# Optimization experiments

Measured on AMD Instinct MI355X. Metric: run time of the kernel, lower is better.

The kernel has to match this reference:

```python
import jax, jax.numpy as jnp
import numpy as np
from jax import lax

Z_DIM = 64
ZS_SIZE = [[1, 1]] * 12 + [[2, 1]] + [[2, 2]] * 11 + [[4, 2]] + [[4, 4]] * 11  # 36 embeddings
FILTER = [[16, 16]] * 6 + [[16, 32]] + [[32, 32]] * 5 + [[32, 64]] + [[64, 64]] * 5  # 18 blocks
OFFS = np.cumsum([0] + [h * k for h, k in ZS_SIZE]).tolist()  # 242 z-vectors total


def _hyper(Z, hn_w2, hn_b2, hn_w1, hn_b1):
    # Batched HyperNetwork: Z [n, 64] -> kernels [n, 16, 16, 3, 3]
    n = Z.shape[0]
    h_in = (Z @ hn_w2 + hn_b2).reshape(n, 16, Z_DIM)            # [n, 16, 64]
    h_fin = jnp.einsum('nid,do->nio', h_in, hn_w1) + hn_b1       # [n, 16, 144]
    return h_fin.reshape(n, 16, 16, 3, 3)


def _make_w(z_all, idx, hn_w2, hn_b2, hn_w1, hn_b1):
    # Assemble conv weight [h*16, k*16, 3, 3] from h*k hypernet tiles (cat dim=1 over k, dim=0 over h)
    h, k = ZS_SIZE[idx]
    Z = z_all[OFFS[idx]:OFFS[idx] + h * k]
    K = _hyper(Z, hn_w2, hn_b2, hn_w1, hn_b1)                    # [h*k, 16, 16, 3, 3]
    K = K.reshape(h, k, 16, 16, 3, 3).transpose(0, 2, 1, 3, 4, 5)
    return K.reshape(h * 16, k * 16, 3, 3)


def _conv(x, w, stride, pad):
    return lax.conv_general_dilated(x, w, (stride, stride), [(pad, pad), (pad, pad)],
                                    dimension_numbers=('NCHW', 'OIHW', 'NCHW'))


def _bn(x, i, g, b, m, v):
    # eval-mode BatchNorm2d with running stats; params padded to 64 channels
    C = x.shape[1]
    gg = g[i, :C].reshape(1, C, 1, 1)
    bb = b[i, :C].reshape(1, C, 1, 1)
    mm = m[i, :C].reshape(1, C, 1, 1)
    vv = v[i, :C].reshape(1, C, 1, 1)
    return (x - mm) * (gg * lax.rsqrt(vv + 1e-5)) + bb


def setup_inputs() -> dict:
    key = jax.random.key(0)
    ks = jax.random.split(key, 16)
    B = 1024
    x = jax.random.normal(ks[0], (B, 3, 32, 32), jnp.float32)
    conv1_w = jax.random.normal(ks[1], (16, 3, 3, 3), jnp.float32) / np.float32(np.sqrt(27.0))
    conv1_b = jnp.zeros((16,), jnp.float32)
    n_bn = 37  # bn1 + 2 per block
    bn_gamma = jnp.ones((n_bn, 64), jnp.float32)
    bn_beta = jnp.zeros((n_bn, 64), jnp.float32)
    bn_mean = jnp.zeros((n_bn, 64), jnp.float32)
    bn_var = jnp.ones((n_bn, 64), jnp.float32)
    hn_w2 = jax.random.normal(ks[2], (Z_DIM, 16 * Z_DIM), jnp.float32) * 0.04
    hn_b2 = jax.random.normal(ks[3], (16 * Z_DIM,), jnp.float32) * 0.01
    hn_w1 = jax.random.normal(ks[4], (Z_DIM, 16 * 9), jnp.float32) * 0.04
    hn_b1 = jax.random.normal(ks[5], (16 * 9,), jnp.float32) * 0.01
    z_all = jax.random.normal(ks[6], (OFFS[-1], Z_DIM), jnp.float32)
    res_w6 = jax.random.normal(ks[7], (32, 16, 1, 1), jnp.float32) * 0.25
    res_b6 = jnp.zeros((32,), jnp.float32)
    res_w12 = jax.random.normal(ks[8], (64, 32, 1, 1), jnp.float32) * 0.18
    res_b12 = jnp.zeros((64,), jnp.float32)
    fin_w = jax.random.normal(ks[9], (10, 64), jnp.float32) * 0.1
    fin_b = jnp.zeros((10,), jnp.float32)
    return {"x": x, "conv1_w": conv1_w, "conv1_b": conv1_b,
            "bn_gamma": bn_gamma, "bn_beta": bn_beta, "bn_mean": bn_mean, "bn_var": bn_var,
            "hn_w2": hn_w2, "hn_b2": hn_b2, "hn_w1": hn_w1, "hn_b1": hn_b1,
            "z_all": z_all, "res_w6": res_w6, "res_b6": res_b6,
            "res_w12": res_w12, "res_b12": res_b12, "fin_w": fin_w, "fin_b": fin_b}


def reference(x, conv1_w, conv1_b, bn_gamma, bn_beta, bn_mean, bn_var,
              hn_w2, hn_b2, hn_w1, hn_b1, z_all,
              res_w6, res_b6, res_w12, res_b12, fin_w, fin_b):
    x = _conv(x, conv1_w, 1, 1) + conv1_b.reshape(1, -1, 1, 1)
    x = jax.nn.relu(_bn(x, 0, bn_gamma, bn_beta, bn_mean, bn_var))
    for i in range(18):
        w1 = _make_w(z_all, 2 * i, hn_w2, hn_b2, hn_w1, hn_b1)
        w2 = _make_w(z_all, 2 * i + 1, hn_w2, hn_b2, hn_w1, hn_b1)
        down = (i > 5 and i % 6 == 0)
        if down:
            rw, rb = (res_w6, res_b6) if i == 6 else (res_w12, res_b12)
            res = _conv(x, rw, 2, 0) + rb.reshape(1, -1, 1, 1)
            stride = 2
        else:
            res = x
            stride = 1
        out = jax.nn.relu(_bn(_conv(x, w1, stride, 1), 1 + 2 * i, bn_gamma, bn_beta, bn_mean, bn_var))
        out = _bn(_conv(out, w2, 1, 1), 2 + 2 * i, bn_gamma, bn_beta, bn_mean, bn_var)
        x = jax.nn.relu(out + res)
    x = x.mean(axis=(2, 3))  # AvgPool2d(8) on [B,64,8,8]
    return x @ fin_w.T + fin_b
```

## Files before the change

### kernel.cpp

```cpp
#include <hip/hip_runtime.h>
#include <hip/hip_bf16.h>


typedef __attribute__((ext_vector_type(8))) short bf16x8;
typedef __attribute__((ext_vector_type(4))) float f32x4;
typedef __attribute__((ext_vector_type(16))) float f32x16;
typedef unsigned short ushort_t;

#define OFFS_LIST {0,1,2,3,4,5,6,7,8,9,10,11,12,14,18,22,26,30,34,38,42,46,50,54,58,66,82,98,114,130,146,162,178,194,210,226,242}
#define K_LIST    {1,1,1,1,1,1,1,1,1,1,1,1,1,2,2,2,2,2,2,2,2,2,2,2,2,4,4,4,4,4,4,4,4,4,4,4}
#define H_LIST    {1,1,1,1,1,1,1,1,1,1,1,1,2,2,2,2,2,2,2,2,2,2,2,2,4,4,4,4,4,4,4,4,4,4,4,4}
#define WOFF_LIST {0,2304,4608,6912,9216,11520,13824,16128,18432,20736,23040,25344,27648,32256,41472,50688,59904,69120,78336,87552,96768,105984,115200,124416,133632,152064,188928,225792,262656,299520,336384,373248,410112,446976,483840,520704}
#define CIN_LIST  {16,16,16,16,16,16,16,16,16,16,16,16,16,32,32,32,32,32,32,32,32,32,32,32,32,64,64,64,64,64,64,64,64,64,64,64}
#define COUT_LIST {16,16,16,16,16,16,16,16,16,16,16,16,32,32,32,32,32,32,32,32,32,32,32,32,64,64,64,64,64,64,64,64,64,64,64,64}
#define WFOFF_LIST {0,7680,15360,23040,30720,38400,46080,53760,61440,69120,76800,84480,92160,107520,139776,170496,201216,231936,262656,293376,324096,354816,385536,416256,446976,508416,637440,760320,883200,1006080,1128960,1251840,1374720,1497600,1620480,1743360}

__constant__ int d_offs[37]  = OFFS_LIST;
__constant__ int d_k[36]     = K_LIST;
__constant__ int d_hh[36]    = H_LIST;
__constant__ int d_woff[36]  = WOFF_LIST;
__constant__ int d_cin[36]   = CIN_LIST;
__constant__ int d_cout[36]  = COUT_LIST;
__constant__ int d_wfoff[36] = WFOFF_LIST;

__device__ inline void split3(float x, ushort_t& h, ushort_t& m, ushort_t& l) {
    unsigned xb = __float_as_uint(x);
    unsigned hb = (xb + 0x8000u) >> 16;
    float fh = __uint_as_float(hb << 16);
    float r = x - fh;
    unsigned mb = (__float_as_uint(r) + 0x8000u) >> 16;
    float fm = __uint_as_float(mb << 16);
    float r2 = r - fm;
    unsigned lb = (__float_as_uint(r2) + 0x8000u) >> 16;
    h = (ushort_t)hb; m = (ushort_t)mb; l = (ushort_t)lb;
}
__device__ inline float b2f(ushort_t u) { return __uint_as_float(((unsigned)u) << 16); }

__device__ inline int swz_bid() {
    int nb = gridDim.x;
    int q = nb >> 3;
    return (blockIdx.x & 7) * q + (blockIdx.x >> 3);
}

__global__ void prep(const float* __restrict__ g, const float* __restrict__ be,
                     const float* __restrict__ m, const float* __restrict__ v,
                     const float* __restrict__ rb6, const float* __restrict__ rb12,
                     float* __restrict__ sc, float* __restrict__ sh,
                     float* __restrict__ shp13, float* __restrict__ shp25) {
    int i = blockIdx.x * blockDim.x + threadIdx.x;
    if (i < 2368) {
        float s = g[i] * rsqrtf(v[i] + 1e-5f);
        sc[i] = s;
        sh[i] = be[i] - m[i] * s;
    } else if (i < 2368 + 32) {
        int c = i - 2368;
        int idx2 = 14 * 64 + c;
        float s = g[idx2] * rsqrtf(v[idx2] + 1e-5f);
        shp13[c] = be[idx2] - m[idx2] * s + rb6[c];
    } else if (i < 2400 + 64) {
        int c = i - 2400;
        int idx2 = 26 * 64 + c;
        float s = g[idx2] * rsqrtf(v[idx2] + 1e-5f);
        shp25[c] = be[idx2] - m[idx2] * s + rb12[c];
    }
}

__global__ void hyper_kernel(const float* __restrict__ z_all, const float* __restrict__ w2,
                             const float* __restrict__ b2, const float* __restrict__ w1,
                             const float* __restrict__ b1, const float* __restrict__ bnsc,
                             float* __restrict__ Wg) {
    int n = blockIdx.x;
    int tid = threadIdx.x;
    __shared__ float zrow[64];
    __shared__ float hin[1024];
    if (tid < 64) zrow[tid] = z_all[n * 64 + tid];
    __syncthreads();
    for (int mcol = tid; mcol < 1024; mcol += 256) {
        float acc = b2[mcol];
        #pragma unroll 8
        for (int d = 0; d < 64; ++d) acc += zrow[d] * w2[d * 1024 + mcol];
        hin[mcol] = acc;
    }
    __syncthreads();
    int L = 0;
    while (n >= d_offs[L + 1]) ++L;
    int r = n - d_offs[L];
    int kk = d_k[L];
    int a = r / kk, bb = r % kk;
    int Cin = kk * 16;
    int Cout = d_hh[L] * 16;
    const float* scp = bnsc + (L + 1) * 64;
    float* wp = Wg + d_woff[L];
    for (int e = tid; e < 2304; e += 256) {
        int i = e / 144, o = e % 144;
        int j = o / 9, tap = o % 9;
        float acc = b1[o];
        #pragma unroll 8
        for (int d = 0; d < 64; ++d) acc += hin[i * 64 + d] * w1[d * 144 + o];
        int co = a * 16 + i;
        acc *= scp[co];
        wp[(tap * Cin + (bb * 16 + j)) * Cout + co] = acc;
    }
}

__global__ void split_w(const float* __restrict__ Wg, const float* __restrict__ rw6,
                        const float* __restrict__ rw12, ushort_t* __restrict__ Wf) {
    int L = blockIdx.y;
    int CIN = d_cin[L], COUT = d_cout[L];
    int idx = blockIdx.x * 256 + threadIdx.x;
    int j = idx & 7, lane = (idx >> 3) & 63, t = idx >> 9;
    int hi = lane >> 5;
    float wv;
    int base;
    if (L < 13) {
        int K = 9 * CIN, NKS = (K + 31) / 32, NT = COUT / 16;
        if (t >= NKS * NT) return;
        int nt = t % NT, ks = t / NT;
        int k = ks * 32 + (lane >> 4) * 8 + j;
        int co = nt * 16 + (lane & 15);
        wv = (k < K) ? Wg[d_woff[L] + k * COUT + co] : 0.f;
        base = d_wfoff[L] + ((ks * NT + nt) * 3) * 512 + lane * 8 + j;
    } else {
        int CG8 = CIN / 8, NKS = 5 * CG8, NT = COUT / 32;
        int TKS = NKS + ((L == 25) ? 2 : ((L == 13) ? 1 : 0));
        if (t >= TKS * NT) return;
        int nt = t % NT, ks = t / NT;
        int co = nt * 32 + (lane & 31);
        if (ks < NKS) {
            int o = 2 * ks + hi, tap = o % 10, c8 = o / 10;
            int ci = c8 * 8 + j;
            wv = (tap < 9) ? Wg[d_woff[L] + (tap * CIN + ci) * COUT + co] : 0.f;
        } else if (L == 25) {
            int k = (ks - NKS) * 16 + hi * 8 + j;
            wv = rw12[co * 32 + k];
        } else {
            int k = hi * 8 + j;
            wv = rw6[co * 16 + k];
        }
        base = d_wfoff[L] + ((ks * NT + nt) * 3) * 512 + lane * 8 + j;
    }
    ushort_t h, m, l;
    split3(wv, h, m, l);
    Wf[base] = h; Wf[base + 512] = m; Wf[base + 1024] = l;
}

__global__ void conv_first(const float* __restrict__ x, const float* __restrict__ cw,
                           const float* __restrict__ cb, const float* __restrict__ g,
                           const float* __restrict__ be, const float* __restrict__ m,
                           const float* __restrict__ v, float* __restrict__ out) {
    int idx = swz_bid() * 256 + threadIdx.x;
    int px = idx & 31; int t = idx >> 5;
    int py = t & 31;   int b = t >> 5;
    float acc[16];
    #pragma unroll
    for (int co = 0; co < 16; ++co) acc[co] = 0.f;
    const float* ip = x + (long)b * 3 * 1024;
    #pragma unroll 1
    for (int ci = 0; ci < 3; ++ci) {
        #pragma unroll 1
        for (int ky = 0; ky < 3; ++ky) {
            int iy = py + ky - 1;
            if ((unsigned)iy >= 32u) continue;
            #pragma unroll
            for (int kx = 0; kx < 3; ++kx) {
                int ix = px + kx - 1;
                if ((unsigned)ix < 32u) {
                    float xv = ip[ci * 1024 + iy * 32 + ix];
                    #pragma unroll
                    for (int co = 0; co < 16; ++co)
                        acc[co] += xv * cw[co * 27 + ci * 9 + ky * 3 + kx];
                }
            }
        }
    }
    long o = ((long)(b * 32 + py) * 32 + px) * 16;
    #pragma unroll
    for (int co = 0; co < 16; ++co) {
        float s = g[co] * rsqrtf(v[co] + 1e-5f);
        float val = (acc[co] + cb[co] - m[co]) * s + be[co];
        out[o + co] = fmaxf(val, 0.f);
    }
}

__global__ void pad_zero_f32(float* __restrict__ buf, int H2, int C4) {
    int idx = blockIdx.x * 256 + threadIdx.x;
    int nb = 2 * H2 + 2 * (H2 - 2);
    int total = 1024 * nb * C4;
    if (idx >= total) return;
    int ch = idx % C4; int t = idx / C4;
    int bp = t % nb; int img = t / nb;
    int y, x;
    if (bp < H2) { y = 0; x = bp; }
    else if (bp < 2 * H2) { y = H2 - 1; x = bp - H2; }
    else { int s = bp - 2 * H2; y = 1 + (s >> 1); x = (s & 1) ? H2 - 1 : 0; }
    long off = (((long)img * H2 + y) * H2 + x) * (C4 * 4) + ch * 4;
    *(float4*)(buf + off) = make_float4(0.f, 0.f, 0.f, 0.f);
}

template<int MODE>
__global__ __launch_bounds__(256) void conv_s1(
        const float* __restrict__ in, const ushort_t* __restrict__ wf,
        const float* __restrict__ shp, const float* __restrict__ res,
        float* __restrict__ out) {
    constexpr int W2 = 34, SLABPIX = 10 * W2;
    constexpr int NKS = 5;

    __shared__ uint4 lds[6 * SLABPIX];

    int tid = threadIdx.x, lane = tid & 63, wid = tid >> 6;
    int g = lane >> 4, r16 = lane & 15;
    int bid = swz_bid();
    int img = bid >> 2, blocky = bid & 3;
    int row0 = blocky * 8;

    const ushort_t* wfl = wf + lane * 8;
    bf16x8 wv[NKS][3];
    #pragma unroll
    for (int ks = 0; ks < NKS; ++ks)
        #pragma unroll
        for (int p = 0; p < 3; ++p)
            wv[ks][p] = *(const bf16x8*)(wfl + (ks * 3 + p) * 512);
    #pragma unroll
    for (int ks = 0; ks < NKS; ++ks)
        #pragma unroll
        for (int p = 0; p < 3; ++p)
            asm volatile("" : "+v"(wv[ks][p]));

    const float* ib = in + (long)img * (32 * 32 * 16);
    for (int it = tid; it < SLABPIX * 2; it += 256) {
        int pix = it % SLABPIX, cc = it / SLABPIX;
        int sr = pix / W2, sc = pix % W2;
        int gy = row0 - 1 + sr, gx = sc - 1;
        float vv[8];
        if ((unsigned)gy < 32u && (unsigned)gx < 32u) {
            const float4* p4 = (const float4*)(ib + ((long)gy * 32 + gx) * 16 + cc * 8);
            float4 a0 = p4[0], a1 = p4[1];
            vv[0]=a0.x; vv[1]=a0.y; vv[2]=a0.z; vv[3]=a0.w;
            vv[4]=a1.x; vv[5]=a1.y; vv[6]=a1.z; vv[7]=a1.w;
        } else {
            #pragma unroll
            for (int q = 0; q < 8; ++q) vv[q] = 0.f;
        }
        union { ushort_t u[8]; uint4 q; } H, M, L;
        #pragma unroll
        for (int q = 0; q < 8; ++q) split3(vv[q], H.u[q], M.u[q], L.u[q]);
        lds[(cc * 3 + 0) * SLABPIX + pix] = H.q;
        lds[(cc * 3 + 1) * SLABPIX + pix] = M.q;
        lds[(cc * 3 + 2) * SLABPIX + pix] = L.q;
    }
    __syncthreads();

    int pbase[4];
    #pragma unroll
    for (int mt = 0; mt < 4; ++mt) {
        int pid = (wid * 4 + mt) * 16 + r16;
        pbase[mt] = (pid >> 5) * W2 + (pid & 31);
    }

    f32x4 acc[4] = {};

    __builtin_amdgcn_s_setprio(1);
    #pragma unroll
    for (int ks = 0; ks < NKS; ++ks) {
        int k0 = ks * 32 + g * 8;
        int tap = k0 >> 4;
        int ci8 = (k0 >> 3) & 1;
        int ky = (tap * 11) >> 5;
        int kx = tap - 3 * ky;
        bool dead = (ks == NKS - 1) && (g >= 2);
        int ofs = dead ? 0 : (ci8 * 3) * SLABPIX + ky * W2 + kx;
        #pragma unroll
        for (int mt = 0; mt < 4; ++mt) {
            int e16 = dead ? 0 : ofs + pbase[mt];
            bf16x8 ah = *(const bf16x8*)&lds[e16];
            bf16x8 am = *(const bf16x8*)&lds[e16 + SLABPIX];
            bf16x8 al = *(const bf16x8*)&lds[e16 + 2 * SLABPIX];
            f32x4 c = acc[mt];
            c = __builtin_amdgcn_mfma_f32_16x16x32_bf16(ah, wv[ks][0], c, 0, 0, 0);
            c = __builtin_amdgcn_mfma_f32_16x16x32_bf16(ah, wv[ks][1], c, 0, 0, 0);
            c = __builtin_amdgcn_mfma_f32_16x16x32_bf16(am, wv[ks][0], c, 0, 0, 0);
            c = __builtin_amdgcn_mfma_f32_16x16x32_bf16(ah, wv[ks][2], c, 0, 0, 0);
            c = __builtin_amdgcn_mfma_f32_16x16x32_bf16(am, wv[ks][1], c, 0, 0, 0);
            c = __builtin_amdgcn_mfma_f32_16x16x32_bf16(al, wv[ks][0], c, 0, 0, 0);
            acc[mt] = c;
        }
    }
    __builtin_amdgcn_s_setprio(0);

    #pragma unroll
    for (int mt = 0; mt < 4; ++mt) {
        #pragma unroll
        for (int reg = 0; reg < 4; ++reg) {
            int pid = (wid * 4 + mt) * 16 + g * 4 + reg;
            int gy = row0 + (pid >> 5), gx = pid & 31;
            long oidx = (((long)img * 32 + gy) * 32 + gx) * 16 + r16;
            float val = acc[mt][reg] + shp[r16];
            if (MODE == 1) val += res[oidx];
            out[oidx] = fmaxf(val, 0.f);
        }
    }
}

template<int CIN, int COUT, int HIN, int STRIDE, int TH, int TW, int OUTF>
__global__ __launch_bounds__(256) void conv_mfma(
        const float* __restrict__ in, const ushort_t* __restrict__ wf,
        const float* __restrict__ shp, float* __restrict__ out) {
    constexpr int HOUT = HIN / STRIDE;
    constexpr int H2O = HOUT + 2;
    constexpr int CG8 = CIN / 8;
    constexpr int IH = (TH - 1) * STRIDE + 3;
    constexpr int IW = (TW - 1) * STRIDE + 3;
    constexpr int K = 9 * CIN;
    constexpr int NKS = (K + 31) / 32;
    constexpr bool TAIL = (K % 32) != 0;
    constexpr int NT = COUT / 16;
    constexpr int MTW = TH * TW / 64;
    constexpr int PADC = ((2 - (IH * IW)) % 8 + 8) % 8;
    constexpr int CSTU = IH * IW + PADC;
    constexpr int PST = CG8 * CSTU;
    constexpr int TX = HOUT / TW, TY = HOUT / TH;

    __shared__ uint4 lds[3 * PST];

    int tid = threadIdx.x;
    int bid = swz_bid();
    int tile = bid % (TY * TX);
    int b = bid / (TY * TX);
    int ty = tile / TX, tx = tile % TX;
    int Y0 = ty * TH, X0 = tx * TW;
    int gy0 = Y0 * STRIDE - 1, gx0 = X0 * STRIDE - 1;

    for (int e = tid; e < CG8 * IH * IW; e += 256) {
        int c8 = e / (IH * IW); int rr = e % (IH * IW);
        int ly = rr / IW, lx = rr % IW;
        int gy = gy0 + ly, gx = gx0 + lx;
        float vv[8];
        if ((unsigned)gy < (unsigned)HIN && (unsigned)gx < (unsigned)HIN) {
            const float4* p = (const float4*)(in + ((long)(b * HIN + gy) * HIN + gx) * CIN + c8 * 8);
            float4 a0 = p[0], a1 = p[1];
            vv[0]=a0.x; vv[1]=a0.y; vv[2]=a0.z; vv[3]=a0.w;
            vv[4]=a1.x; vv[5]=a1.y; vv[6]=a1.z; vv[7]=a1.w;
        } else {
            #pragma unroll
            for (int q = 0; q < 8; ++q) vv[q] = 0.f;
        }
        union { ushort_t u[8]; uint4 q4; } H, M, L;
        #pragma unroll
        for (int q = 0; q < 8; ++q) split3(vv[q], H.u[q], M.u[q], L.u[q]);
        int a16 = c8 * CSTU + rr;
        lds[a16] = H.q4; lds[PST + a16] = M.q4; lds[2 * PST + a16] = L.q4;
    }
    __syncthreads();

    int lane = tid & 63, wid = tid >> 6;
    int g = lane >> 4, r16 = lane & 15;

    f32x4 acc[MTW][NT] = {};

    int pbase[MTW];
    #pragma unroll
    for (int mt = 0; mt < MTW; ++mt) {
        int pid = (wid + 4 * mt) * 16 + r16;
        int py = pid / TW, px = pid % TW;
        pbase[mt] = (py * STRIDE) * IW + px * STRIDE;
    }

    __builtin_amdgcn_s_setprio(1);
    #pragma unroll
    for (int ks = 0; ks < NKS; ++ks) {
        bf16x8 bfr[NT][3];
        #pragma unroll
        for (int nt = 0; nt < NT; ++nt)
            #pragma unroll
            for (int p = 0; p < 3; ++p)
                bfr[nt][p] = *(const bf16x8*)(wf + ((ks * NT + nt) * 3 + p) * 512 + lane * 8);

        int k0 = ks * 32 + g * 8;
        int tap = k0 / CIN;
        int ci8 = (k0 % CIN) >> 3;
        int ky = (tap * 11) >> 5;
        int kx = tap - 3 * ky;
        int ofs = ci8 * CSTU + ky * IW + kx;

        #pragma unroll
        for (int mt = 0; mt < MTW; ++mt) {
            int e16 = ofs + pbase[mt];
            if (TAIL && ks == NKS - 1) e16 = (g < 2) ? e16 : 0;
            const uint4* ap = lds + e16;
            bf16x8 ah = *(const bf16x8*)(ap);
            bf16x8 am = *(const bf16x8*)(ap + PST);
            bf16x8 al = *(const bf16x8*)(ap + 2 * PST);
            #pragma unroll
            for (int nt = 0; nt < NT; ++nt) {
                f32x4 c = acc[mt][nt];
                c = __builtin_amdgcn_mfma_f32_16x16x32_bf16(ah, bfr[nt][0], c, 0, 0, 0);
                c = __builtin_amdgcn_mfma_f32_16x16x32_bf16(ah, bfr[nt][1], c, 0, 0, 0);
                c = __builtin_amdgcn_mfma_f32_16x16x32_bf16(am, bfr[nt][0], c, 0, 0, 0);
                c = __builtin_amdgcn_mfma_f32_16x16x32_bf16(ah, bfr[nt][2], c, 0, 0, 0);
                c = __builtin_amdgcn_mfma_f32_16x16x32_bf16(am, bfr[nt][1], c, 0, 0, 0);
                c = __builtin_amdgcn_mfma_f32_16x16x32_bf16(al, bfr[nt][0], c, 0, 0, 0);
                acc[mt][nt] = c;
            }
        }
    }
    __builtin_amdgcn_s_setprio(0);

    #pragma unroll
    for (int mt = 0; mt < MTW; ++mt) {
        #pragma unroll
        for (int nt = 0; nt < NT; ++nt) {
            int co = nt * 16 + r16;
            float shv = shp[co];
            #pragma unroll
            for (int reg = 0; reg < 4; ++reg) {
                int pid = (wid + 4 * mt) * 16 + g * 4 + reg;
                int py = pid / TW, px = pid % TW;
                int gy = Y0 + py, gx = X0 + px;
                float val = fmaxf(acc[mt][nt][reg] + shv, 0.f);
                if (OUTF == 0) {
                    out[((long)(b * HOUT + gy) * HOUT + gx) * COUT + co] = val;
                } else {
                    out[(((long)b * H2O + gy + 1) * H2O + gx + 1) * COUT + co] = val;
                }
            }
        }
    }
}

template<int CIN, int COUT, int HIN, int STRIDE, int PXB, int MODE, int RKS, int CHUNK>
__global__ __launch_bounds__(256) void conv_s23(
        const float* __restrict__ in, const ushort_t* __restrict__ wf,
        const float* __restrict__ shp, const float* __restrict__ res,
        float* __restrict__ out) {
    constexpr int HOUT = HIN / STRIDE;
    constexpr int H2I = HIN + 2, H2O = HOUT + 2;
    constexpr int C8 = CIN / 8;
    constexpr int NKS = 5 * C8;
    constexpr int TKS = NKS + RKS;
    constexpr int NC = TKS / CHUNK;
    constexpr int NTT = COUT / 32;
    constexpr int ROWSB = PXB / HOUT;
    constexpr int SLABR = (ROWSB - 1) * STRIDE + 3;
    constexpr int SLABPIX = SLABR * H2I;
    constexpr int NBLK = HOUT / ROWSB;
    constexpr int RESU = 3 * C8 * SLABPIX;
    constexpr int LDSU = RESU + ((MODE == 2 || MODE == 3) ? 768 : 0);

    __shared__ uint4 lds[LDSU];

    int tid = threadIdx.x, lane = tid & 63, wid = tid >> 6;
    int lp = lane & 31, hi = lane >> 5;
    int bid = swz_bid();
    int img = bid / NBLK, blocky = bid % NBLK;
    int pxg = wid / NTT, ntb = wid % NTT;
    int pix0 = pxg * 32 + lp;
    int py_blk = pix0 / HOUT, px = pix0 % HOUT;
    int py = blocky * ROWSB + py_blk;
    int slabrow0 = blocky * ROWSB * STRIDE;

    const ushort_t* wfl = wf + lane * 8;

    bf16x8 wA[CHUNK][3], wB[CHUNK][3];
    auto LW = [&](int c, bf16x8 (&w)[CHUNK][3]) {
        #pragma unroll
        for (int i = 0; i < CHUNK; ++i) {
            int ks = c * CHUNK + i;
            #pragma unroll
            for (int pp = 0; pp < 3; ++pp)
                w[i][pp] = *(const bf16x8*)(wfl + ((ks * NTT + ntb) * 3 + pp) * 512);
        }
    };

    LW(0, wA);
    if (NC > 1) LW(1, wB);

    const float* ib = in + (long)img * H2I * H2I * CIN;
    for (int it = tid; it < SLABPIX * C8; it += 256) {
        int pix = it % SLABPIX, cc = it / SLABPIX;
        int sr = pix / H2I, sc = pix % H2I;
        const float* p4 = ib + ((long)(slabrow0 + sr) * H2I + sc) * CIN + cc * 8;
        float4 a0 = ((const float4*)p4)[0], a1 = ((const float4*)p4)[1];
        float vv[8] = {a0.x, a0.y, a0.z, a0.w, a1.x, a1.y, a1.z, a1.w};
        union { ushort_t u[8]; uint4 q; } H, M, L;
        #pragma unroll
        for (int q = 0; q < 8; ++q) split3(vv[q], H.u[q], M.u[q], L.u[q]);
        int u0 = cc * 3;
        lds[u0 * SLABPIX + pix] = H.q;
        lds[(u0 + 1) * SLABPIX + pix] = M.q;
        lds[(u0 + 2) * SLABPIX + pix] = L.q;
    }
    if (MODE == 2) {
        for (int it = tid; it < 256; it += 256) {
            int pix = it & 63, cc = it >> 6;
            int ry = pix >> 3, rx = pix & 7;
            const float* r4 = res + (((long)img * 18 + (2 * ry + 1)) * 18 + (2 * rx + 1)) * 32 + cc * 8;
            float4 a0 = ((const float4*)r4)[0], a1 = ((const float4*)r4)[1];
            float vv[8] = {a0.x, a0.y, a0.z, a0.w, a1.x, a1.y, a1.z, a1.w};
            union { ushort_t u[8]; uint4 q; } H, M, L;
            #pragma unroll
            for (int q = 0; q < 8; ++q) split3(vv[q], H.u[q], M.u[q], L.u[q]);
            int u0 = RESU + cc * 3 * 64;
            lds[u0 + pix] = H.q;
            lds[u0 + 64 + pix] = M.q;
            lds[u0 + 128 + pix] = L.q;
        }
    }
    if (MODE == 3) {
        for (int it = tid; it < 256; it += 256) {
            int opix = it >> 1, cg = it & 1;
            int r = opix / 16, cxx = opix % 16;
            int gy = (blocky * 8 + r) * 2, gx = cxx * 2;
            const float* r4 = res + (((long)img * 32 + gy) * 32 + gx) * 16 + cg * 8;
            float4 a0 = ((const float4*)r4)[0], a1 = ((const float4*)r4)[1];
            float vv[8] = {a0.x, a0.y, a0.z, a0.w, a1.x, a1.y, a1.z, a1.w};
            union { ushort_t u[8]; uint4 q; } H, M, L;
            #pragma unroll
            for (int q = 0; q < 8; ++q) split3(vv[q], H.u[q], M.u[q], L.u[q]);
            int u0 = RESU + opix * 6;
            lds[u0 + cg] = H.q;
            lds[u0 + 2 + cg] = M.q;
            lds[u0 + 4 + cg] = L.q;
        }
    }
    __syncthreads();

    int pbase = (py_blk * STRIDE) * H2I + px * STRIDE;
    f32x16 acc = {};

    auto DOC = [&](int c, bf16x8 (&w)[CHUNK][3]) {
        #pragma unroll
        for (int i = 0; i < CHUNK; ++i) {
            int ks = c * CHUNK + i;
            bf16x8 x0, x1, x2;
            if (RKS > 0 && ks >= NKS) {
                if (MODE == 2) {
                    int o2 = 2 * (ks - NKS) + hi;
                    int a = RESU + o2 * 3 * 64 + pix0;
                    x0 = *(const bf16x8*)&lds[a];
                    x1 = *(const bf16x8*)&lds[a + 64];
                    x2 = *(const bf16x8*)&lds[a + 128];
                } else {
                    int a = RESU + pix0 * 6 + hi;
                    x0 = *(const bf16x8*)&lds[a];
                    x1 = *(const bf16x8*)&lds[a + 2];
                    x2 = *(const bf16x8*)&lds[a + 4];
                }
            } else {
                int o = 2 * ks + hi;
                int tap = o % 10, c8i = o / 10;
                int ky = (tap * 11) >> 5, kx = tap - 3 * ky;
                int t16 = (tap == 9) ? 0 : (ky * H2I + kx);
                int a = (c8i * 3) * SLABPIX + pbase + t16;
                x0 = *(const bf16x8*)&lds[a];
                x1 = *(const bf16x8*)&lds[a + SLABPIX];
                x2 = *(const bf16x8*)&lds[a + 2 * SLABPIX];
            }
            acc = __builtin_amdgcn_mfma_f32_32x32x16_bf16(w[i][0], x0, acc, 0, 0, 0);
            acc = __builtin_amdgcn_mfma_f32_32x32x16_bf16(w[i][1], x0, acc, 0, 0, 0);
            acc = __builtin_amdgcn_mfma_f32_32x32x16_bf16(w[i][0], x1, acc, 0, 0, 0);
            acc = __builtin_amdgcn_mfma_f32_32x32x16_bf16(w[i][2], x0, acc, 0, 0, 0);
            acc = __builtin_amdgcn_mfma_f32_32x32x16_bf16(w[i][1], x1, acc, 0, 0, 0);
            acc = __builtin_amdgcn_mfma_f32_32x32x16_bf16(w[i][0], x2, acc, 0, 0, 0);
        }
    };

    __builtin_amdgcn_s_setprio(1);
    #pragma unroll 1
    for (int c = 0; c < NC; c += 2) {
        DOC(c, wA);
        if (c + 2 < NC) LW(c + 2, wA);
        if (c + 1 < NC) { DOC(c + 1, wB); if (c + 3 < NC) LW(c + 3, wB); }
    }
    __builtin_amdgcn_s_setprio(0);

    float* ob = out + (((long)img * H2O + py + 1) * H2O + (px + 1)) * COUT;
    #pragma unroll
    for (int g = 0; g < 4; ++g) {
        int co = ntb * 32 + g * 8 + 4 * hi;
        float v0 = acc[4 * g + 0] + shp[co + 0];
        float v1 = acc[4 * g + 1] + shp[co + 1];
        float v2 = acc[4 * g + 2] + shp[co + 2];
        float v3 = acc[4 * g + 3] + shp[co + 3];
        *(float4*)(ob + co) = make_float4(fmaxf(v0, 0.f), fmaxf(v1, 0.f),
                                          fmaxf(v2, 0.f), fmaxf(v3, 0.f));
    }
}

template<int CIN, int HIN, int TPW, int BLK>
__global__ __launch_bounds__(BLK) void block_fused(
        const float* __restrict__ in, const ushort_t* __restrict__ wf1,
        const ushort_t* __restrict__ wf2, const float* __restrict__ sh1,
        const float* __restrict__ sh2, float* __restrict__ out) {
    constexpr int H2 = HIN + 2, H2PIX = H2 * H2;
    constexpr int C8 = CIN / 8;
    constexpr int NKS = 5 * C8;
    constexpr int CHUNK = 5, NC = NKS / CHUNK;
    constexpr int NTT = CIN / 32;
    constexpr int BUFU = 3 * C8 * H2PIX;

    __shared__ uint4 lds[BUFU];
    ushort_t* lsh = (ushort_t*)lds;

    int tid = threadIdx.x, lane = tid & 63, wid = tid >> 6;
    int lp = lane & 31, hi = lane >> 5;
    int img = swz_bid();

    int ntb0 = (wid * TPW) % NTT;
    int pb[TPW];
    #pragma unroll
    for (int t = 0; t < TPW; ++t) {
        int tl = wid * TPW + t;
        int pix = (tl / NTT) * 32 + lp;
        pb[t] = (pix / HIN + 1) * H2 + (pix % HIN + 1);
    }

    const float* ib = in + (long)img * H2PIX * CIN;
    for (int it = tid; it < H2PIX * C8; it += BLK) {
        int cc = it % C8, pix = it / C8;
        const float4* p4 = (const float4*)(ib + (long)pix * CIN + cc * 8);
        float4 a0 = p4[0], a1 = p4[1];
        float vv[8] = {a0.x, a0.y, a0.z, a0.w, a1.x, a1.y, a1.z, a1.w};
        union { ushort_t u[8]; uint4 q; } H, M, L;
        #pragma unroll
        for (int q = 0; q < 8; ++q) split3(vv[q], H.u[q], M.u[q], L.u[q]);
        lds[(cc * 3 + 0) * H2PIX + pix] = H.q;
        lds[(cc * 3 + 1) * H2PIX + pix] = M.q;
        lds[(cc * 3 + 2) * H2PIX + pix] = L.q;
    }
    __syncthreads();

    bf16x8 wA[CHUNK][3], wB[CHUNK][3];
    f32x16 acc[TPW];

    auto CONV = [&](const ushort_t* wf) {
        const ushort_t* wfl = wf + lane * 8;
        #pragma unroll
        for (int t = 0; t < TPW; ++t)
            #pragma unroll
            for (int q = 0; q < 16; ++q) acc[t][q] = 0.f;
        auto LW = [&](int c, bf16x8 (&w)[CHUNK][3]) {
            #pragma unroll
            for (int i = 0; i < CHUNK; ++i) {
                int ks = c * CHUNK + i;
                #pragma unroll
                for (int pp = 0; pp < 3; ++pp)
                    w[i][pp] = *(const bf16x8*)(wfl + ((ks * NTT + ntb0) * 3 + pp) * 512);
            }
        };
        auto DOC = [&](int c, bf16x8 (&w)[CHUNK][3]) {
            #pragma unroll
            for (int i = 0; i < CHUNK; ++i) {
                int ks = c * CHUNK + i;
                int o = 2 * ks + hi;
                int tap = o % 10, c8i = o / 10;
                int ky = (tap * 11) >> 5, kx = tap - 3 * ky;
                int rel = (tap == 9) ? 0 : (ky - 1) * H2 + (kx - 1);
                #pragma unroll
                for (int t = 0; t < TPW; ++t) {
                    int a = (tap == 9) ? (c8i * 3) * H2PIX
                                       : (c8i * 3) * H2PIX + pb[t] + rel;
                    bf16x8 x0 = *(const bf16x8*)&lds[a];
                    bf16x8 x1 = *(const bf16x8*)&lds[a + H2PIX];
                    bf16x8 x2 = *(const bf16x8*)&lds[a + 2 * H2PIX];
                    f32x16 c2 = acc[t];
                    c2 = __builtin_amdgcn_mfma_f32_32x32x16_bf16(w[i][0], x0, c2, 0, 0, 0);
                    c2 = __builtin_amdgcn_mfma_f32_32x32x16_bf16(w[i][1], x0, c2, 0, 0, 0);
                    c2 = __builtin_amdgcn_mfma_f32_32x32x16_bf16(w[i][0], x1, c2, 0, 0, 0);
                    c2 = __builtin_amdgcn_mfma_f32_32x32x16_bf16(w[i][2], x0, c2, 0, 0, 0);
                    c2 = __builtin_amdgcn_mfma_f32_32x32x16_bf16(w[i][1], x1, c2, 0, 0, 0);
                    c2 = __builtin_amdgcn_mfma_f32_32x32x16_bf16(w[i][0], x2, c2, 0, 0, 0);
                    acc[t] = c2;
                }
            }
        };
        LW(0, wA);
        if (NC > 1) LW(1, wB);
        __builtin_amdgcn_s_setprio(1);
        #pragma unroll 1
        for (int c = 0; c < NC; c += 2) {
            DOC(c, wA);
            if (c + 2 < NC) LW(c + 2, wA);
            if (c + 1 < NC) { DOC(c + 1, wB); if (c + 3 < NC) LW(c + 3, wB); }
        }
        __builtin_amdgcn_s_setprio(0);
    };

    CONV(wf1);
    __syncthreads();
    #pragma unroll
    for (int t = 0; t < TPW; ++t) {
        #pragma unroll
        for (int q = 0; q < 4; ++q) {
            int co = ntb0 * 32 + q * 8 + 4 * hi;
            int c8o = co >> 3;
            ushort4 h4, m4, l4;
            #pragma unroll
            for (int e = 0; e < 4; ++e) {
                float val = fmaxf(acc[t][4 * q + e] + sh1[co + e], 0.f);
                ushort_t h, m2, l;
                split3(val, h, m2, l);
                ((ushort_t*)&h4)[e] = h; ((ushort_t*)&m4)[e] = m2; ((ushort_t*)&l4)[e] = l;
            }
            int so = (((c8o * 3) * H2PIX + pb[t]) << 3) + (co & 7);
            *(ushort4*)&lsh[so] = h4;
            *(ushort4*)&lsh[so + H2PIX * 8] = m4;
            *(ushort4*)&lsh[so + 2 * H2PIX * 8] = l4;
        }
    }
    __syncthreads();

    CONV(wf2);
    float* ob = out + (long)img * H2PIX * CIN;
    #pragma unroll
    for (int t = 0; t < TPW; ++t) {
        #pragma unroll
        for (int q = 0; q < 4; ++q) {
            int co = ntb0 * 32 + q * 8 + 4 * hi;
            float4 r = *(const float4*)(ib + (long)pb[t] * CIN + co);
            float v0 = acc[t][4 * q + 0] + sh2[co + 0] + r.x;
            float v1 = acc[t][4 * q + 1] + sh2[co + 1] + r.y;
            float v2 = acc[t][4 * q + 2] + sh2[co + 2] + r.z;
            float v3 = acc[t][4 * q + 3] + sh2[co + 3] + r.w;
            *(float4*)(ob + (long)pb[t] * CIN + co) =
                make_float4(fmaxf(v0, 0.f), fmaxf(v1, 0.f), fmaxf(v2, 0.f), fmaxf(v3, 0.f));
        }
    }
}

__global__ void pool_fc(const float* __restrict__ X, const float* __restrict__ fw,
                        const float* __restrict__ fb, float* __restrict__ out) {
    int b = blockIdx.x;
    int c = threadIdx.x;
    float s = 0.f;
    #pragma unroll
    for (int p = 0; p < 64; ++p) {
        int y = p >> 3, x = p & 7;
        s += X[(((long)b * 10 + y + 1) * 10 + (x + 1)) * 64 + c];
    }
    __shared__ float pooled[64];
    pooled[c] = s * (1.f / 64.f);
    __syncthreads();
    if (c < 10) {
        float acc = fb[c];
        #pragma unroll
        for (int k = 0; k < 64; ++k) acc += pooled[k] * fw[c * 64 + k];
        out[b * 10 + c] = acc;
    }
}

extern "C" void kernel_launch(void* const* d_in, const int* in_sizes, int n_in,
                              void* d_out, int out_size, void* d_ws, size_t ws_size,
                              hipStream_t stream) {
    const float* x       = (const float*)d_in[0];
    const float* conv1_w = (const float*)d_in[1];
    const float* conv1_b = (const float*)d_in[2];
    const float* bn_g    = (const float*)d_in[3];
    const float* bn_b    = (const float*)d_in[4];
    const float* bn_m    = (const float*)d_in[5];
    const float* bn_v    = (const float*)d_in[6];
    const float* hn_w2   = (const float*)d_in[7];
    const float* hn_b2   = (const float*)d_in[8];
    const float* hn_w1   = (const float*)d_in[9];
    const float* hn_b1   = (const float*)d_in[10];
    const float* z_all   = (const float*)d_in[11];
    const float* res_w6  = (const float*)d_in[12];
    const float* res_b6  = (const float*)d_in[13];
    const float* res_w12 = (const float*)d_in[14];
    const float* res_b12 = (const float*)d_in[15];
    const float* fin_w   = (const float*)d_in[16];
    const float* fin_b   = (const float*)d_in[17];
    float* outp = (float*)d_out;

    float* wsf      = (float*)d_ws;
    float* Wg       = wsf;
    float* bnsc     = wsf + 557568;
    float* bnsh     = wsf + 559936;
    float* shp13    = wsf + 562304;
    float* shp25    = wsf + 564864;
    ushort_t* Wfrag = (ushort_t*)(wsf + 565248);

    float* A0f = (float*)((char*)d_ws + (size_t)(16) * (1 << 20));
    float* A1f = (float*)((char*)d_ws + (size_t)(80) * (1 << 20));
    float* A2f = (float*)((char*)d_ws + (size_t)(144) * (1 << 20));

    static const int wfoff[36] = WFOFF_LIST;

    prep<<<20, 256, 0, stream>>>(bn_g, bn_b, bn_m, bn_v, res_b6, res_b12,
                                 bnsc, bnsh, shp13, shp25);
    hyper_kernel<<<242, 256, 0, stream>>>(z_all, hn_w2, hn_b2, hn_w1, hn_b1, bnsc, Wg);
    split_w<<<dim3(168, 36), 256, 0, stream>>>(Wg, res_w6, res_w12, Wfrag);
    conv_first<<<4096, 256, 0, stream>>>(x, conv1_w, conv1_b, bn_g, bn_b, bn_m, bn_v, A0f);

    float* X = A0f; float* T1 = A1f; float* T2 = A2f;
    for (int i = 0; i < 6; ++i) {
        int L1 = 2 * i, L2 = 2 * i + 1;
        conv_s1<0><<<4096, 256, 0, stream>>>(
            X, Wfrag + wfoff[L1], bnsh + (L1 + 1) * 64, nullptr, T1);
        conv_s1<1><<<4096, 256, 0, stream>>>(
            T1, Wfrag + wfoff[L2], bnsh + (L2 + 1) * 64, X, T2);
        float* tmp = X; X = T2; T2 = tmp;
    }
    pad_zero_f32<<<2176, 256, 0, stream>>>(A1f, 18, 8);
    conv_mfma<16,32,32,2,8,16,1><<<2048, 256, 0, stream>>>(
        A0f, Wfrag + wfoff[12], bnsh + 13 * 64, A1f);
    pad_zero_f32<<<2176, 256, 0, stream>>>(A2f, 18, 8);
    conv_s23<32,32,16,1,128,3,1,3><<<2048, 256, 0, stream>>>(
        A1f, Wfrag + wfoff[13], shp13, A0f, A2f);

    X = A2f; float* T = A1f;
    for (int i = 7; i < 12; ++i) {
        int L1 = 2 * i, L2 = 2 * i + 1;
        block_fused<32,16,2,256><<<1024, 256, 0, stream>>>(
            X, Wfrag + wfoff[L1], Wfrag + wfoff[L2],
            bnsh + (L1 + 1) * 64, bnsh + (L2 + 1) * 64, T);
        float* tmp = X; X = T; T = tmp;
    }
    pad_zero_f32<<<2304, 256, 0, stream>>>(A0f, 10, 16);
    conv_s23<32,64,16,2,64,0,0,5><<<1024, 256, 0, stream>>>(
        A1f, Wfrag + wfoff[24], bnsh + 25 * 64, nullptr, A0f);
    pad_zero_f32<<<2304, 256, 0, stream>>>(A2f, 10, 16);
    conv_s23<64,64,8,1,64,2,2,6><<<1024, 256, 0, stream>>>(
        A0f, Wfrag + wfoff[25], shp25, A1f, A2f);

    X = A2f; T = A0f;
    for (int i = 13; i < 18; ++i) {
        int L1 = 2 * i, L2 = 2 * i + 1;
        block_fused<64,8,1,256><<<1024, 256, 0, stream>>>(
            X, Wfrag + wfoff[L1], Wfrag + wfoff[L2],
            bnsh + (L1 + 1) * 64, bnsh + (L2 + 1) * 64, T);
        float* tmp = X; X = T; T = tmp;
    }
    pool_fc<<<1024, 64, 0, stream>>>(A0f, fin_w, fin_b, outp);
}
```

Baseline: 1.276 ms.

## Store stage-2/3 activations as pre-split bf16x3 planes between fused blocks

```diff
diff --git a/kernel.cpp b/kernel.cpp
--- a/kernel.cpp
+++ b/kernel.cpp
@@ -197,6 +197,22 @@
     *(float4*)(buf + off) = make_float4(0.f, 0.f, 0.f, 0.f);
 }
 
+__global__ void pad_zero_pl(ushort_t* __restrict__ buf, int H2, int C8) {
+    int idx = blockIdx.x * 256 + threadIdx.x;
+    int nb = 4 * H2 - 4;
+    int U = C8 * 3;
+    int total = 1024 * nb * U;
+    if (idx >= total) return;
+    int u = idx % U; int t = idx / U;
+    int bp = t % nb; int img = t / nb;
+    int y, x;
+    if (bp < H2) { y = 0; x = bp; }
+    else if (bp < 2 * H2) { y = H2 - 1; x = bp - H2; }
+    else { int s = bp - 2 * H2; y = 1 + (s >> 1); x = (s & 1) ? H2 - 1 : 0; }
+    long unit = ((long)img * U + u) * (H2 * H2) + y * H2 + x;
+    ((uint4*)buf)[unit] = make_uint4(0, 0, 0, 0);
+}
+
 template<int MODE>
 __global__ __launch_bounds__(256) void conv_s1(
         const float* __restrict__ in, const ushort_t* __restrict__ wf,
@@ -427,14 +443,17 @@
     }
 }
 
-template<int CIN, int COUT, int HIN, int STRIDE, int PXB, int MODE, int RKS, int CHUNK>
+template<int CIN, int COUT, int HIN, int STRIDE, int PXB, int MODE, int RKS,
+         int CHUNK, int INF, int OUTF>
 __global__ __launch_bounds__(256) void conv_s23(
-        const float* __restrict__ in, const ushort_t* __restrict__ wf,
-        const float* __restrict__ shp, const float* __restrict__ res,
-        float* __restrict__ out) {
+        const float* __restrict__ inf32, const ushort_t* __restrict__ inpl,
+        const ushort_t* __restrict__ wf, const float* __restrict__ shp,
+        const float* __restrict__ resf32, const ushort_t* __restrict__ respl,
+        float* __restrict__ outf32, ushort_t* __restrict__ outpl) {
     constexpr int HOUT = HIN / STRIDE;
     constexpr int H2I = HIN + 2, H2O = HOUT + 2;
     constexpr int C8 = CIN / 8;
+    constexpr int C8O = COUT / 8;
     constexpr int NKS = 5 * C8;
     constexpr int TKS = NKS + RKS;
     constexpr int NC = TKS / CHUNK;
@@ -474,35 +493,40 @@
     LW(0, wA);
     if (NC > 1) LW(1, wB);
 
-    const float* ib = in + (long)img * H2I * H2I * CIN;
-    for (int it = tid; it < SLABPIX * C8; it += 256) {
-        int pix = it % SLABPIX, cc = it / SLABPIX;
-        int sr = pix / H2I, sc = pix % H2I;
-        const float* p4 = ib + ((long)(slabrow0 + sr) * H2I + sc) * CIN + cc * 8;
-        float4 a0 = ((const float4*)p4)[0], a1 = ((const float4*)p4)[1];
-        float vv[8] = {a0.x, a0.y, a0.z, a0.w, a1.x, a1.y, a1.z, a1.w};
-        union { ushort_t u[8]; uint4 q; } H, M, L;
-        #pragma unroll
-        for (int q = 0; q < 8; ++q) split3(vv[q], H.u[q], M.u[q], L.u[q]);
-        int u0 = cc * 3;
-        lds[u0 * SLABPIX + pix] = H.q;
-        lds[(u0 + 1) * SLABPIX + pix] = M.q;
-        lds[(u0 + 2) * SLABPIX + pix] = L.q;
+    if (INF == 0) {
+        const float* ib = inf32 + (long)img * H2I * H2I * CIN;
+        for (int it = tid; it < SLABPIX * C8; it += 256) {
+            int pix = it % SLABPIX, cc = it / SLABPIX;
+            int sr = pix / H2I, sc = pix % H2I;
+            const float* p4 = ib + ((long)(slabrow0 + sr) * H2I + sc) * CIN + cc * 8;
+            float4 a0 = ((const float4*)p4)[0], a1 = ((const float4*)p4)[1];
+            float vv[8] = {a0.x, a0.y, a0.z, a0.w, a1.x, a1.y, a1.z, a1.w};
+            union { ushort_t u[8]; uint4 q; } H, M, L;
+            #pragma unroll
+            for (int q = 0; q < 8; ++q) split3(vv[q], H.u[q], M.u[q], L.u[q]);
+            int u0 = cc * 3;
+            lds[u0 * SLABPIX + pix] = H.q;
+            lds[(u0 + 1) * SLABPIX + pix] = M.q;
+            lds[(u0 + 2) * SLABPIX + pix] = L.q;
+        }
+    } else {
+        const uint4* gp = (const uint4*)inpl;
+        for (int it = tid; it < C8 * 3 * SLABPIX; it += 256) {
+            int u = it / SLABPIX, pix = it % SLABPIX;
+            lds[u * SLABPIX + pix] =
+                gp[((long)img * C8 * 3 + u) * (H2I * H2I) + slabrow0 * H2I + pix];
+        }
     }
     if (MODE == 2) {
+        const uint4* gr = (const uint4*)respl;
         for (int it = tid; it < 256; it += 256) {
             int pix = it & 63, cc = it >> 6;
             int ry = pix >> 3, rx = pix & 7;
-            const float* r4 = res + (((long)img * 18 + (2 * ry + 1)) * 18 + (2 * rx + 1)) * 32 + cc * 8;
-            float4 a0 = ((const float4*)r4)[0], a1 = ((const float4*)r4)[1];
-            float vv[8] = {a0.x, a0.y, a0.z, a0.w, a1.x, a1.y, a1.z, a1.w};
-            union { ushort_t u[8]; uint4 q; } H, M, L;
-            #pragma unroll
-            for (int q = 0; q < 8; ++q) split3(vv[q], H.u[q], M.u[q], L.u[q]);
-            int u0 = RESU + cc * 3 * 64;
-            lds[u0 + pix] = H.q;
-            lds[u0 + 64 + pix] = M.q;
-            lds[u0 + 128 + pix] = L.q;
+            int rpix = (2 * ry + 1) * 18 + (2 * rx + 1);
+            #pragma unroll
+            for (int p = 0; p < 3; ++p)
+                lds[RESU + (cc * 3 + p) * 64 + pix] =
+                    gr[((long)img * 12 + cc * 3 + p) * 324 + rpix];
         }
     }
     if (MODE == 3) {
@@ -510,7 +534,7 @@
             int opix = it >> 1, cg = it & 1;
             int r = opix / 16, cxx = opix % 16;
             int gy = (blocky * 8 + r) * 2, gx = cxx * 2;
-            const float* r4 = res + (((long)img * 32 + gy) * 32 + gx) * 16 + cg * 8;
+            const float* r4 = resf32 + (((long)img * 32 + gy) * 32 + gx) * 16 + cg * 8;
             float4 a0 = ((const float4*)r4)[0], a1 = ((const float4*)r4)[1];
             float vv[8] = {a0.x, a0.y, a0.z, a0.w, a1.x, a1.y, a1.z, a1.w};
             union { ushort_t u[8]; uint4 q; } H, M, L;
@@ -573,32 +597,47 @@
     }
     __builtin_amdgcn_s_setprio(0);
 
-    float* ob = out + (((long)img * H2O + py + 1) * H2O + (px + 1)) * COUT;
-    #pragma unroll
-    for (int g = 0; g < 4; ++g) {
-        int co = ntb * 32 + g * 8 + 4 * hi;
-        float v0 = acc[4 * g + 0] + shp[co + 0];
-        float v1 = acc[4 * g + 1] + shp[co + 1];
-        float v2 = acc[4 * g + 2] + shp[co + 2];
-        float v3 = acc[4 * g + 3] + shp[co + 3];
-        *(float4*)(ob + co) = make_float4(fmaxf(v0, 0.f), fmaxf(v1, 0.f),
-                                          fmaxf(v2, 0.f), fmaxf(v3, 0.f));
+    int opix = (py + 1) * H2O + (px + 1);
+    #pragma unroll
+    for (int q = 0; q < 4; ++q) {
+        int co = ntb * 32 + q * 8 + 4 * hi;
+        float v[4];
+        #pragma unroll
+        for (int e = 0; e < 4; ++e) v[e] = fmaxf(acc[4 * q + e] + shp[co + e], 0.f);
+        if (OUTF == 0) {
+            float* ob = outf32 + ((long)img * H2O * H2O + opix) * COUT;
+            *(float4*)(ob + co) = make_float4(v[0], v[1], v[2], v[3]);
+        } else {
+            int c8o = co >> 3;
+            ushort4 h4, m4, l4;
+            #pragma unroll
+            for (int e = 0; e < 4; ++e) {
+                ushort_t h, m2, l;
+                split3(v[e], h, m2, l);
+                ((ushort_t*)&h4)[e] = h; ((ushort_t*)&m4)[e] = m2; ((ushort_t*)&l4)[e] = l;
+            }
+            long so = (((long)img * C8O * 3 + c8o * 3) * (H2O * H2O) + opix) * 8 + 4 * hi;
+            long ps = (long)(H2O * H2O) * 8;
+            *(ushort4*)&outpl[so] = h4;
+            *(ushort4*)&outpl[so + ps] = m4;
+            *(ushort4*)&outpl[so + 2 * ps] = l4;
+        }
     }
 }
 
 template<int CIN, int HIN, int TPW, int BLK>
 __global__ __launch_bounds__(BLK) void block_fused(
-        const float* __restrict__ in, const ushort_t* __restrict__ wf1,
+        const ushort_t* __restrict__ in, const ushort_t* __restrict__ wf1,
         const ushort_t* __restrict__ wf2, const float* __restrict__ sh1,
-        const float* __restrict__ sh2, float* __restrict__ out) {
+        const float* __restrict__ sh2, ushort_t* __restrict__ out) {
     constexpr int H2 = HIN + 2, H2PIX = H2 * H2;
     constexpr int C8 = CIN / 8;
     constexpr int NKS = 5 * C8;
     constexpr int CHUNK = 5, NC = NKS / CHUNK;
     constexpr int NTT = CIN / 32;
-    constexpr int BUFU = 3 * C8 * H2PIX;
-
-    __shared__ uint4 lds[BUFU];
+    constexpr int NU = 3 * C8 * H2PIX;
+
+    __shared__ uint4 lds[NU];
     ushort_t* lsh = (ushort_t*)lds;
 
     int tid = threadIdx.x, lane = tid & 63, wid = tid >> 6;
@@ -614,19 +653,8 @@
         pb[t] = (pix / HIN + 1) * H2 + (pix % HIN + 1);
     }
 
-    const float* ib = in + (long)img * H2PIX * CIN;
-    for (int it = tid; it < H2PIX * C8; it += BLK) {
-        int cc = it % C8, pix = it / C8;
-        const float4* p4 = (const float4*)(ib + (long)pix * CIN + cc * 8);
-        float4 a0 = p4[0], a1 = p4[1];
-        float vv[8] = {a0.x, a0.y, a0.z, a0.w, a1.x, a1.y, a1.z, a1.w};
-        union { ushort_t u[8]; uint4 q; } H, M, L;
-        #pragma unroll
-        for (int q = 0; q < 8; ++q) split3(vv[q], H.u[q], M.u[q], L.u[q]);
-        lds[(cc * 3 + 0) * H2PIX + pix] = H.q;
-        lds[(cc * 3 + 1) * H2PIX + pix] = M.q;
-        lds[(cc * 3 + 2) * H2PIX + pix] = L.q;
-    }
+    const uint4* gp = (const uint4*)in + (long)img * NU;
+    for (int it = tid; it < NU; it += BLK) lds[it] = gp[it];
     __syncthreads();
 
     bf16x8 wA[CHUNK][3], wB[CHUNK][3];
@@ -686,7 +714,24 @@
     };
 
     CONV(wf1);
+    float resv[TPW][4][4];
+    #pragma unroll
+    for (int t = 0; t < TPW; ++t) {
+        #pragma unroll
+        for (int q = 0; q < 4; ++q) {
+            int c8o = ntb0 * 4 + q;
+            int b0 = ((c8o * 3) * H2PIX + pb[t]) * 8 + 4 * hi;
+            ushort4 rh = *(const ushort4*)&lsh[b0];
+            ushort4 rm = *(const ushort4*)&lsh[b0 + H2PIX * 8];
+            ushort4 rl = *(const ushort4*)&lsh[b0 + 2 * H2PIX * 8];
+            resv[t][q][0] = b2f(rh.x) + b2f(rm.x) + b2f(rl.x);
+            resv[t][q][1] = b2f(rh.y) + b2f(rm.y) + b2f(rl.y);
+            resv[t][q][2] = b2f(rh.z) + b2f(rm.z) + b2f(rl.z);
+            resv[t][q][3] = b2f(rh.w) + b2f(rm.w) + b2f(rl.w);
+        }
+    }
     __syncthreads();
+
     #pragma unroll
     for (int t = 0; t < TPW; ++t) {
         #pragma unroll
@@ -701,7 +746,7 @@
                 split3(val, h, m2, l);
                 ((ushort_t*)&h4)[e] = h; ((ushort_t*)&m4)[e] = m2; ((ushort_t*)&l4)[e] = l;
             }
-            int so = (((c8o * 3) * H2PIX + pb[t]) << 3) + (co & 7);
+            int so = ((c8o * 3) * H2PIX + pb[t]) * 8 + (co & 7);
             *(ushort4*)&lsh[so] = h4;
             *(ushort4*)&lsh[so + H2PIX * 8] = m4;
             *(ushort4*)&lsh[so + 2 * H2PIX * 8] = l4;
@@ -710,32 +755,43 @@
     __syncthreads();
 
     CONV(wf2);
-    float* ob = out + (long)img * H2PIX * CIN;
+    ushort_t* op = out + (long)img * NU * 8;
     #pragma unroll
     for (int t = 0; t < TPW; ++t) {
         #pragma unroll
         for (int q = 0; q < 4; ++q) {
             int co = ntb0 * 32 + q * 8 + 4 * hi;
-            float4 r = *(const float4*)(ib + (long)pb[t] * CIN + co);
-            float v0 = acc[t][4 * q + 0] + sh2[co + 0] + r.x;
-            float v1 = acc[t][4 * q + 1] + sh2[co + 1] + r.y;
-            float v2 = acc[t][4 * q + 2] + sh2[co + 2] + r.z;
-            float v3 = acc[t][4 * q + 3] + sh2[co + 3] + r.w;
-            *(float4*)(ob + (long)pb[t] * CIN + co) =
-                make_float4(fmaxf(v0, 0.f), fmaxf(v1, 0.f), fmaxf(v2, 0.f), fmaxf(v3, 0.f));
-        }
-    }
-}
-
-__global__ void pool_fc(const float* __restrict__ X, const float* __restrict__ fw,
+            int c8o = co >> 3;
+            ushort4 h4, m4, l4;
+            #pragma unroll
+            for (int e = 0; e < 4; ++e) {
+                float val = fmaxf(acc[t][4 * q + e] + sh2[co + e] + resv[t][q][e], 0.f);
+                ushort_t h, m2, l;
+                split3(val, h, m2, l);
+                ((ushort_t*)&h4)[e] = h; ((ushort_t*)&m4)[e] = m2; ((ushort_t*)&l4)[e] = l;
+            }
+            long so = ((long)(c8o * 3) * H2PIX + pb[t]) * 8 + (co & 7);
+            *(ushort4*)&op[so] = h4;
+            *(ushort4*)&op[so + (long)H2PIX * 8] = m4;
+            *(ushort4*)&op[so + (long)2 * H2PIX * 8] = l4;
+        }
+    }
+}
+
+__global__ void pool_fc(const ushort_t* __restrict__ X, const float* __restrict__ fw,
                         const float* __restrict__ fb, float* __restrict__ out) {
     int b = blockIdx.x;
     int c = threadIdx.x;
+    int c8 = c >> 3, el = c & 7;
+    const ushort_t* ib = X + (long)b * 19200;
     float s = 0.f;
     #pragma unroll
     for (int p = 0; p < 64; ++p) {
         int y = p >> 3, x = p & 7;
-        s += X[(((long)b * 10 + y + 1) * 10 + (x + 1)) * 64 + c];
+        int pix = (y + 1) * 10 + (x + 1);
+        #pragma unroll
+        for (int pl = 0; pl < 3; ++pl)
+            s += b2f(ib[((c8 * 3 + pl) * 100 + pix) * 8 + el]);
     }
     __shared__ float pooled[64];
     pooled[c] = s * (1.f / 64.f);
@@ -782,6 +838,9 @@
     float* A0f = (float*)((char*)d_ws + (size_t)(16) * (1 << 20));
     float* A1f = (float*)((char*)d_ws + (size_t)(80) * (1 << 20));
     float* A2f = (float*)((char*)d_ws + (size_t)(144) * (1 << 20));
+    ushort_t* A0s = (ushort_t*)A0f;
+    ushort_t* A1s = (ushort_t*)A1f;
+    ushort_t* A2s = (ushort_t*)A2f;
 
     static const int wfoff[36] = WFOFF_LIST;
 
@@ -803,32 +862,34 @@
     pad_zero_f32<<<2176, 256, 0, stream>>>(A1f, 18, 8);
     conv_mfma<16,32,32,2,8,16,1><<<2048, 256, 0, stream>>>(
         A0f, Wfrag + wfoff[12], bnsh + 13 * 64, A1f);
-    pad_zero_f32<<<2176, 256, 0, stream>>>(A2f, 18, 8);
-    conv_s23<32,32,16,1,128,3,1,3><<<2048, 256, 0, stream>>>(
-        A1f, Wfrag + wfoff[13], shp13, A0f, A2f);
-
-    X = A2f; float* T = A1f;
+    pad_zero_pl<<<3264, 256, 0, stream>>>(A2s, 18, 4);
+    conv_s23<32,32,16,1,128,3,1,3,0,1><<<2048, 256, 0, stream>>>(
+        A1f, nullptr, Wfrag + wfoff[13], shp13, A0f, nullptr, nullptr, A2s);
+    pad_zero_pl<<<3264, 256, 0, stream>>>(A1s, 18, 4);
+
+    ushort_t* Xs = A2s; ushort_t* Ts = A1s;
     for (int i = 7; i < 12; ++i) {
         int L1 = 2 * i, L2 = 2 * i + 1;
         block_fused<32,16,2,256><<<1024, 256, 0, stream>>>(
-            X, Wfrag + wfoff[L1], Wfrag + wfoff[L2],
-            bnsh + (L1 + 1) * 64, bnsh + (L2 + 1) * 64, T);
-        float* tmp = X; X = T; T = tmp;
+            Xs, Wfrag + wfoff[L1], Wfrag + wfoff[L2],
+            bnsh + (L1 + 1) * 64, bnsh + (L2 + 1) * 64, Ts);
+        ushort_t* tmp = Xs; Xs = Ts; Ts = tmp;
     }
     pad_zero_f32<<<2304, 256, 0, stream>>>(A0f, 10, 16);
-    conv_s23<32,64,16,2,64,0,0,5><<<1024, 256, 0, stream>>>(
-        A1f, Wfrag + wfoff[24], bnsh + 25 * 64, nullptr, A0f);
-    pad_zero_f32<<<2304, 256, 0, stream>>>(A2f, 10, 16);
-    conv_s23<64,64,8,1,64,2,2,6><<<1024, 256, 0, stream>>>(
-        A0f, Wfrag + wfoff[25], shp25, A1f, A2f);
-
-    X = A2f; T = A0f;
+    conv_s23<32,64,16,2,64,0,0,5,1,0><<<1024, 256, 0, stream>>>(
+        nullptr, A1s, Wfrag + wfoff[24], bnsh + 25 * 64, nullptr, nullptr, A0f, nullptr);
+    pad_zero_pl<<<3456, 256, 0, stream>>>(A2s, 10, 8);
+    conv_s23<64,64,8,1,64,2,2,6,0,1><<<1024, 256, 0, stream>>>(
+        A0f, nullptr, Wfrag + wfoff[25], shp25, nullptr, A1s, nullptr, A2s);
+    pad_zero_pl<<<3456, 256, 0, stream>>>(A0s, 10, 8);
+
+    Xs = A2s; Ts = A0s;
     for (int i = 13; i < 18; ++i) {
         int L1 = 2 * i, L2 = 2 * i + 1;
         block_fused<64,8,1,256><<<1024, 256, 0, stream>>>(
-            X, Wfrag + wfoff[L1], Wfrag + wfoff[L2],
-            bnsh + (L1 + 1) * 64, bnsh + (L2 + 1) * 64, T);
-        float* tmp = X; X = T; T = tmp;
-    }
-    pool_fc<<<1024, 64, 0, stream>>>(A0f, fin_w, fin_b, outp);
-}
+            Xs, Wfrag + wfoff[L1], Wfrag + wfoff[L2],
+            bnsh + (L1 + 1) * 64, bnsh + (L2 + 1) * 64, Ts);
+        ushort_t* tmp = Xs; Xs = Ts; Ts = tmp;
+    }
+    pool_fc<<<1024, 64, 0, stream>>>(A0s, fin_w, fin_b, outp);
+}
```

After: 1.475 ms. +15.5%, slower.
